# Optimization experiments

Measured on AMD Instinct MI355X. Metric: run time of the kernel, lower is better.

The kernel has to match this reference:

```python
import jax, jax.numpy as jnp
import numpy as np

N = 1024      # num_features
H = 256       # num_hidden_features
E = 64        # embedding_size
HD = 64       # hidden_size
B = 8192


def setup_inputs() -> dict:
    key = jax.random.key(0)
    ks = jax.random.split(key, 7)
    glorot_e = (2.0 / (N + E)) ** 0.5
    glorot_w = (2.0 / (2 * E + HD)) ** 0.5
    glorot_u = (2.0 / (HD + 1)) ** 0.5
    return {
        "values": jax.random.uniform(ks[0], (B, N), dtype=jnp.float32),
        "feat_emb": jax.random.normal(ks[1], (N, E), dtype=jnp.float32) * glorot_e,
        "hid_emb": jax.random.normal(ks[2], (H, E), dtype=jnp.float32) * glorot_e,
        "W_w": jax.random.normal(ks[3], (2 * E, HD), dtype=jnp.float32) * glorot_w,
        "b_w": jnp.zeros((HD,), dtype=jnp.float32),
        "W_u": jax.random.normal(ks[4], (HD, 1), dtype=jnp.float32) * glorot_u,
        "mask": jax.random.bernoulli(ks[5], 0.5, (N, N + H)),
    }


def _forward(values, feat_emb, hid_emb, W_w, b_w, W_u, mask):
    # full embedding table over extended vocab: [M, E], M = N + H
    full = jnp.concatenate([feat_emb, hid_emb], axis=0)
    # Dense w applied to concat([feat_i, full_j]) == split-matmul, avoids [N,M,2E]
    W1, W2 = W_w[:E], W_w[E:]                      # each [E, HD]
    a = feat_emb @ W1                              # [N, HD]
    b = full @ W2                                  # [M, HD]
    h = jnp.tanh(a[:, None, :] + b[None, :, :] + b_w)  # [N, M, HD]
    score = jnp.squeeze(h @ W_u, axis=-1)          # [N, M]
    score = jnp.where(mask, jnp.exp(score), 0.0)
    score_sum = jnp.sum(score, axis=1, keepdims=True)
    score_sum = jnp.where(score_sum == 0, 1.0, score_sum)
    attention_weights = score / score_sum          # [N, M]
    context = attention_weights @ full             # [N, E]
    return values @ context                        # [B, E]


def reference(values, feat_emb, hid_emb, W_w, b_w, W_u, mask):
    return _forward(values, feat_emb, hid_emb, W_w, b_w, W_u, mask)
```

## Files before the change

### kernel.cpp

```cpp
#include <hip/hip_runtime.h>
#include <hip/hip_bf16.h>

#define NF   1024
#define NHID 256
#define NJ   1280
#define ED   64
#define BATCH 8192

#define K2E   2.8853900817779268f
#define LOG2E 1.4426950408889634f

__device__ __forceinline__ float exp2_fast(float x) {
    float r;
    asm("v_exp_f32 %0, %1" : "=v"(r) : "v"(x));
    return r;
}

__global__ __launch_bounds__(256) void prep_kernel(
    const float* __restrict__ feat, const float* __restrict__ hid,
    const float* __restrict__ Ww, const float* __restrict__ bw,
    const float* __restrict__ Wu,
    float* __restrict__ Ap, float* __restrict__ BvT, float* __restrict__ swu)
{
    __shared__ __align__(16) float in_s[64][64];
    __shared__ __align__(16) float tout[64][65];
    const int tid = threadIdx.x;
    const int b   = blockIdx.x;
    const bool isA = (b < 16);
    const int e  = tid & 63;
    const int wv = tid >> 6;

    if (b == 0 && tid < 64) {
        float s = Wu[tid];
        #pragma unroll
        for (int off = 32; off > 0; off >>= 1) s += __shfl_down(s, off);
        if (tid == 0) swu[0] = s * LOG2E;
    }

    const float* W = isA ? Ww : (Ww + 4096);
    float wcol[64];
    #pragma unroll
    for (int k = 0; k < 64; k++) wcol[k] = W[k * 64 + e];
    const float bias = isA ? 0.f : bw[e];

    const int bb = isA ? b : (b - 16);
    const float* src = isA ? (feat + (size_t)bb * 4096)
                     : (bb < 16 ? (feat + (size_t)bb * 4096)
                                : (hid + (size_t)(bb - 16) * 4096));
    #pragma unroll
    for (int s = 0; s < 4; s++)
        ((float4*)&in_s[0][0])[tid + s * 256] = ((const float4*)src)[tid + s * 256];
    __syncthreads();

    float acc[16];
    #pragma unroll
    for (int r = 0; r < 16; r++) acc[r] = bias;
    for (int k4 = 0; k4 < 64; k4 += 4) {
        #pragma unroll
        for (int r = 0; r < 16; r++) {
            float4 iv = *(const float4*)&in_s[wv * 16 + r][k4];
            acc[r] += iv.x*wcol[k4+0] + iv.y*wcol[k4+1] + iv.z*wcol[k4+2] + iv.w*wcol[k4+3];
        }
    }

    if (isA) {
        #pragma unroll
        for (int r = 0; r < 16; r++)
            Ap[(size_t)(b * 64 + wv * 16 + r) * 64 + e] = acc[r] * K2E;
    } else {
        #pragma unroll
        for (int r = 0; r < 16; r++) tout[wv * 16 + r][e] = acc[r] * K2E;
        __syncthreads();
        const int j0 = bb * 64;
        #pragma unroll
        for (int q = 0; q < 4; q++) {
            float4 v;
            v.x = tout[wv * 16 + q * 4 + 0][e];
            v.y = tout[wv * 16 + q * 4 + 1][e];
            v.z = tout[wv * 16 + q * 4 + 2][e];
            v.w = tout[wv * 16 + q * 4 + 3][e];
            *(float4*)&BvT[(size_t)e * NJ + j0 + wv * 16 + q * 4] = v;
        }
    }
}

__global__ __launch_bounds__(256) void score_kernel(
    const float* __restrict__ Wu, const float* __restrict__ Ap,
    const float* __restrict__ BvT, const float* __restrict__ swu,
    const void* __restrict__ maskp, float* __restrict__ sc)
{
    __shared__ int mtype_s;
    const int tid = threadIdx.x;
    const int iq  = blockIdx.x / 5;
    const int jc  = blockIdx.x - iq * 5;
    const int i0  = iq * 4;
    const int j   = jc * 256 + tid;

    if (tid < 64) {
        const unsigned int* mw = (const unsigned int*)maskp;
        unsigned int w = mw[tid];
        unsigned long long notf = __ballot(w != 0u && w != 0x3F800000u);
        unsigned long long gt1  = __ballot(w > 1u);
        if (tid == 0) mtype_s = (notf == 0ull) ? 2 : ((gt1 == 0ull) ? 1 : 0);
    }
    __syncthreads();

    const float* a0p = Ap + (size_t)(i0 + 0) * 64;
    const float* a1p = Ap + (size_t)(i0 + 1) * 64;
    const float* a2p = Ap + (size_t)(i0 + 2) * 64;
    const float* a3p = Ap + (size_t)(i0 + 3) * 64;
    const float* bp  = BvT + j;

    float acc0 = 0.f, acc1 = 0.f, acc2 = 0.f, acc3 = 0.f;
    #pragma unroll 8
    for (int e = 0; e < 64; e++) {
        float b  = bp[(size_t)e * NJ];
        float wu = Wu[e];
        float t, r;
        t = a0p[e] + b; r = __builtin_amdgcn_rcpf(exp2_fast(t) + 1.f); acc0 = fmaf(wu, r, acc0);
        t = a1p[e] + b; r = __builtin_amdgcn_rcpf(exp2_fast(t) + 1.f); acc1 = fmaf(wu, r, acc1);
        t = a2p[e] + b; r = __builtin_amdgcn_rcpf(exp2_fast(t) + 1.f); acc2 = fmaf(wu, r, acc2);
        t = a3p[e] + b; r = __builtin_amdgcn_rcpf(exp2_fast(t) + 1.f); acc3 = fmaf(wu, r, acc3);
    }

    const float SwuL = swu[0];
    const int mtype = mtype_s;
    const unsigned char* m8  = (const unsigned char*)maskp;
    const unsigned int*  m32 = (const unsigned int*)maskp;
    const float*         mfl = (const float*)maskp;
    float av[4] = {acc0, acc1, acc2, acc3};
    #pragma unroll
    for (int i = 0; i < 4; i++) {
        size_t off = (size_t)(i0 + i) * NJ + j;
        bool bm;
        if (mtype == 0)      bm = m8[off]  != 0;
        else if (mtype == 1) bm = m32[off] != 0u;
        else                 bm = mfl[off] != 0.f;
        sc[off] = bm ? exp2_fast(fmaf(-K2E, av[i], SwuL)) : 0.f;
    }
}

__global__ __launch_bounds__(256) void ctx_kernel(
    const float* __restrict__ feat, const float* __restrict__ hid,
    const float* __restrict__ sc, float* __restrict__ ctx)
{
    __shared__ __align__(16) float sc_s[2][NJ];
    __shared__ __align__(16) float red[2][16][64];
    __shared__ float ssum_s[2];
    const int tid = threadIdx.x;
    const int i0  = blockIdx.x * 2;

    #pragma unroll
    for (int rep = 0; rep < 3; rep++) {
        int idx = tid + rep * 256;
        if (idx < 640) {
            int i  = idx / 320;
            int jq = idx - i * 320;
            *(float4*)&sc_s[i][jq * 4] = *(const float4*)&sc[(size_t)(i0 + i) * NJ + jq * 4];
        }
    }
    __syncthreads();
    if (tid < 128) {
        int i = tid >> 6, e = tid & 63;
        float s = 0.f;
        #pragma unroll
        for (int g = 0; g < 20; g++) s += sc_s[i][e + g * 64];
        #pragma unroll
        for (int off = 32; off > 0; off >>= 1) s += __shfl_down(s, off);
        if (e == 0) ssum_s[i] = (s == 0.f) ? 1.f : s;
    }

    const int jg = tid >> 4;
    const int e4 = (tid & 15) * 4;
    float4 c0 = {0.f,0.f,0.f,0.f}, c1 = {0.f,0.f,0.f,0.f};
    for (int it = 0; it < 80; it++) {
        int j = it * 16 + jg;
        const float* fr = (j < NF) ? (feat + (size_t)j * 64)
                                   : (hid  + (size_t)(j - NF) * 64);
        float4 f = *(const float4*)(fr + e4);
        float w0 = sc_s[0][j], w1 = sc_s[1][j];
        c0.x += w0*f.x; c0.y += w0*f.y; c0.z += w0*f.z; c0.w += w0*f.w;
        c1.x += w1*f.x; c1.y += w1*f.y; c1.z += w1*f.z; c1.w += w1*f.w;
    }
    *(float4*)&red[0][jg][e4] = c0;
    *(float4*)&red[1][jg][e4] = c1;
    __syncthreads();
    if (tid < 128) {
        int half = tid >> 6, e = tid & 63;
        float v = 0.f;
        #pragma unroll
        for (int g = 0; g < 16; g++) v += red[half][g][e];
        ctx[(size_t)(i0 + half) * 64 + e] = v / ssum_s[half];
    }
}

__global__ __launch_bounds__(256) void out_mm_kernel(
    const float* __restrict__ values, const float* __restrict__ ctxp,
    float* __restrict__ dst, int atomic_mode)
{
    __shared__ __align__(16) float vsT[64 * 64];
    __shared__ __align__(16) float cs[64][64];
    const int tid = threadIdx.x;
    const int rt  = blockIdx.x >> 3;
    const int kq  = blockIdx.x & 7;
    const int r0  = rt * 64;
    const int tr  = tid >> 4;
    const int tc4 = (tid & 15) * 4;

    float acc[4][4];
    #pragma unroll
    for (int a = 0; a < 4; a++)
        #pragma unroll
        for (int b = 0; b < 4; b++) acc[a][b] = 0.f;

    for (int ch = 0; ch < 2; ch++) {
        const int k0 = kq * 128 + ch * 64;
        __syncthreads();
        #pragma unroll
        for (int s = 0; s < 4; s++) {
            int t   = tid + s * 256;
            int r   = t >> 4;
            int kk4 = (t & 15) * 4;
            float4 g = *(const float4*)&values[(size_t)(r0 + r) * NF + k0 + kk4];
            int p  = (((r >> 2) + (t & 15)) & 15) * 4 + (r & 3);
            vsT[(kk4 + 0) * 64 + p] = g.x;
            vsT[(kk4 + 1) * 64 + p] = g.y;
            vsT[(kk4 + 2) * 64 + p] = g.z;
            vsT[(kk4 + 3) * 64 + p] = g.w;
        }
        #pragma unroll
        for (int s = 0; s < 4; s++) {
            int t  = tid + s * 256;
            int kk = t >> 4;
            int c4 = (t & 15) * 4;
            *(float4*)&cs[kk][c4] = *(const float4*)&ctxp[(size_t)(k0 + kk) * ED + c4];
        }
        __syncthreads();
        #pragma unroll 8
        for (int k = 0; k < 64; k++) {
            float4 av = *(const float4*)&vsT[k * 64 + (((tr + (k >> 2)) & 15) << 2)];
            float4 bv = *(const float4*)&cs[k][tc4];
            acc[0][0] += av.x*bv.x; acc[0][1] += av.x*bv.y; acc[0][2] += av.x*bv.z; acc[0][3] += av.x*bv.w;
            acc[1][0] += av.y*bv.x; acc[1][1] += av.y*bv.y; acc[1][2] += av.y*bv.z; acc[1][3] += av.y*bv.w;
            acc[2][0] += av.z*bv.x; acc[2][1] += av.z*bv.y; acc[2][2] += av.z*bv.z; acc[2][3] += av.z*bv.w;
            acc[3][0] += av.w*bv.x; acc[3][1] += av.w*bv.y; acc[3][2] += av.w*bv.z; acc[3][3] += av.w*bv.w;
        }
    }
    if (atomic_mode) {
        #pragma unroll
        for (int i2 = 0; i2 < 4; i2++) {
            int r = r0 + tr * 4 + i2;
            float* op = dst + (size_t)r * ED + tc4;
            unsafeAtomicAdd(op + 0, acc[i2][0]);
            unsafeAtomicAdd(op + 1, acc[i2][1]);
            unsafeAtomicAdd(op + 2, acc[i2][2]);
            unsafeAtomicAdd(op + 3, acc[i2][3]);
        }
    } else {
        #pragma unroll
        for (int i2 = 0; i2 < 4; i2++) {
            int r = r0 + tr * 4 + i2;
            float* op = dst + ((size_t)kq * BATCH + r) * ED + tc4;
            *(float4*)op = make_float4(acc[i2][0], acc[i2][1], acc[i2][2], acc[i2][3]);
        }
    }
}

__global__ __launch_bounds__(256) void reduce8_kernel(
    const float* __restrict__ part, float* __restrict__ out)
{
    const size_t S = (size_t)BATCH * ED / 4;
    size_t idx = (size_t)blockIdx.x * 256 + threadIdx.x;
    const float4* p = (const float4*)part;
    float4 r = {0.f, 0.f, 0.f, 0.f};
    #pragma unroll
    for (int q = 0; q < 8; q++) {
        float4 a = p[idx + (size_t)q * S];
        r.x += a.x; r.y += a.y; r.z += a.z; r.w += a.w;
    }
    ((float4*)out)[idx] = r;
}

extern "C" void kernel_launch(void* const* d_in, const int* in_sizes, int n_in,
                              void* d_out, int out_size, void* d_ws, size_t ws_size,
                              hipStream_t stream) {
    const float* values = (const float*)d_in[0];
    const float* feat   = (const float*)d_in[1];
    const float* hid    = (const float*)d_in[2];
    const float* Ww     = (const float*)d_in[3];
    const float* bw     = (const float*)d_in[4];
    const float* Wu     = (const float*)d_in[5];
    const void*  mask   = d_in[6];
    float* out = (float*)d_out;

    float* Ap   = (float*)d_ws;
    float* BvT  = Ap + (size_t)NF * 64;
    float* ctx  = BvT + (size_t)ED * NJ;
    float* swu  = ctx + (size_t)NF * 64;
    float* sc   = swu + 64;
    float* part = sc + (size_t)NF * NJ;
    const size_t need = ((size_t)NF*64 + (size_t)ED*NJ + (size_t)NF*64 + 64
                         + (size_t)NF*NJ + (size_t)8*BATCH*ED) * sizeof(float);
    const bool wsmode = ws_size >= need;

    hipLaunchKernelGGL(prep_kernel, dim3(36), dim3(256), 0, stream,
                       feat, hid, Ww, bw, Wu, Ap, BvT, swu);
    hipLaunchKernelGGL(score_kernel, dim3(1280), dim3(256), 0, stream,
                       Wu, Ap, BvT, swu, mask, sc);
    hipLaunchKernelGGL(ctx_kernel, dim3(512), dim3(256), 0, stream,
                       feat, hid, sc, ctx);
    if (wsmode) {
        hipLaunchKernelGGL(out_mm_kernel, dim3(1024), dim3(256), 0, stream,
                           values, ctx, part, 0);
        hipLaunchKernelGGL(reduce8_kernel, dim3(BATCH * ED / 4 / 256), dim3(256), 0, stream,
                           part, out);
    } else {
        hipMemsetAsync(d_out, 0, (size_t)BATCH * ED * sizeof(float), stream);
        hipLaunchKernelGGL(out_mm_kernel, dim3(1024), dim3(256), 0, stream,
                           values, ctx, out, 1);
    }
}
```

Baseline: 146.1 us.

## Retile output matmul to 256x64 blocks with 8x8 register tiles and atomic split-K

The final values@context matmul now uses 256-row tiles with a 64-wide K slice per block and 8x8 per-thread register accumulators, up from 64 rows and 4x4. The split-K partial buffer and separate reduce kernel are removed. Partial sums go straight into the zeroed output with atomic adds across 16 K-splits. This aims to raise arithmetic intensity and drop the extra partial write/read pass and one launch. In exchange it issues more atomics, needs 80KB of shared memory per block (lower occupancy), and uses more registers.

```diff
diff --git a/kernel.cpp b/kernel.cpp
--- a/kernel.cpp
+++ b/kernel.cpp
@@ -196,89 +196,68 @@
 
 __global__ __launch_bounds__(256) void out_mm_kernel(
     const float* __restrict__ values, const float* __restrict__ ctxp,
-    float* __restrict__ dst, int atomic_mode)
-{
-    __shared__ __align__(16) float vsT[64 * 64];
+    float* __restrict__ out)
+{
+    __shared__ __align__(16) float vsT[64 * 256];
     __shared__ __align__(16) float cs[64][64];
     const int tid = threadIdx.x;
-    const int rt  = blockIdx.x >> 3;
-    const int kq  = blockIdx.x & 7;
-    const int r0  = rt * 64;
-    const int tr  = tid >> 4;
-    const int tc4 = (tid & 15) * 4;
-
-    float acc[4][4];
-    #pragma unroll
-    for (int a = 0; a < 4; a++)
-        #pragma unroll
-        for (int b = 0; b < 4; b++) acc[a][b] = 0.f;
-
-    for (int ch = 0; ch < 2; ch++) {
-        const int k0 = kq * 128 + ch * 64;
-        __syncthreads();
-        #pragma unroll
-        for (int s = 0; s < 4; s++) {
-            int t   = tid + s * 256;
-            int r   = t >> 4;
-            int kk4 = (t & 15) * 4;
-            float4 g = *(const float4*)&values[(size_t)(r0 + r) * NF + k0 + kk4];
-            int p  = (((r >> 2) + (t & 15)) & 15) * 4 + (r & 3);
-            vsT[(kk4 + 0) * 64 + p] = g.x;
-            vsT[(kk4 + 1) * 64 + p] = g.y;
-            vsT[(kk4 + 2) * 64 + p] = g.z;
-            vsT[(kk4 + 3) * 64 + p] = g.w;
-        }
-        #pragma unroll
-        for (int s = 0; s < 4; s++) {
-            int t  = tid + s * 256;
-            int kk = t >> 4;
-            int c4 = (t & 15) * 4;
-            *(float4*)&cs[kk][c4] = *(const float4*)&ctxp[(size_t)(k0 + kk) * ED + c4];
-        }
-        __syncthreads();
-        #pragma unroll 8
-        for (int k = 0; k < 64; k++) {
-            float4 av = *(const float4*)&vsT[k * 64 + (((tr + (k >> 2)) & 15) << 2)];
-            float4 bv = *(const float4*)&cs[k][tc4];
-            acc[0][0] += av.x*bv.x; acc[0][1] += av.x*bv.y; acc[0][2] += av.x*bv.z; acc[0][3] += av.x*bv.w;
-            acc[1][0] += av.y*bv.x; acc[1][1] += av.y*bv.y; acc[1][2] += av.y*bv.z; acc[1][3] += av.y*bv.w;
-            acc[2][0] += av.z*bv.x; acc[2][1] += av.z*bv.y; acc[2][2] += av.z*bv.z; acc[2][3] += av.z*bv.w;
-            acc[3][0] += av.w*bv.x; acc[3][1] += av.w*bv.y; acc[3][2] += av.w*bv.z; acc[3][3] += av.w*bv.w;
-        }
-    }
-    if (atomic_mode) {
-        #pragma unroll
-        for (int i2 = 0; i2 < 4; i2++) {
-            int r = r0 + tr * 4 + i2;
-            float* op = dst + (size_t)r * ED + tc4;
-            unsafeAtomicAdd(op + 0, acc[i2][0]);
-            unsafeAtomicAdd(op + 1, acc[i2][1]);
-            unsafeAtomicAdd(op + 2, acc[i2][2]);
-            unsafeAtomicAdd(op + 3, acc[i2][3]);
-        }
-    } else {
-        #pragma unroll
-        for (int i2 = 0; i2 < 4; i2++) {
-            int r = r0 + tr * 4 + i2;
-            float* op = dst + ((size_t)kq * BATCH + r) * ED + tc4;
-            *(float4*)op = make_float4(acc[i2][0], acc[i2][1], acc[i2][2], acc[i2][3]);
-        }
-    }
-}
-
-__global__ __launch_bounds__(256) void reduce8_kernel(
-    const float* __restrict__ part, float* __restrict__ out)
-{
-    const size_t S = (size_t)BATCH * ED / 4;
-    size_t idx = (size_t)blockIdx.x * 256 + threadIdx.x;
-    const float4* p = (const float4*)part;
-    float4 r = {0.f, 0.f, 0.f, 0.f};
-    #pragma unroll
-    for (int q = 0; q < 8; q++) {
-        float4 a = p[idx + (size_t)q * S];
-        r.x += a.x; r.y += a.y; r.z += a.z; r.w += a.w;
-    }
-    ((float4*)out)[idx] = r;
+    const int rt  = blockIdx.x >> 4;
+    const int kq  = blockIdx.x & 15;
+    const int r0  = rt * 256;
+    const int k0  = kq * 64;
+    const int rg  = tid >> 3;
+    const int c8  = (tid & 7) * 8;
+
+    #pragma unroll
+    for (int s = 0; s < 16; s++) {
+        int t  = tid + s * 256;
+        int r  = t >> 4;
+        int kc = t & 15;
+        float4 g = *(const float4*)&values[(size_t)(r0 + r) * NF + k0 + kc * 4];
+        int p = ((((r >> 3) + kc) & 31) << 3) + (r & 7);
+        vsT[(kc * 4 + 0) * 256 + p] = g.x;
+        vsT[(kc * 4 + 1) * 256 + p] = g.y;
+        vsT[(kc * 4 + 2) * 256 + p] = g.z;
+        vsT[(kc * 4 + 3) * 256 + p] = g.w;
+    }
+    #pragma unroll
+    for (int s = 0; s < 4; s++) {
+        int t  = tid + s * 256;
+        int kk = t >> 4;
+        int c4 = (t & 15) * 4;
+        *(float4*)&cs[kk][c4] = *(const float4*)&ctxp[(size_t)(k0 + kk) * ED + c4];
+    }
+    __syncthreads();
+
+    float acc[8][8];
+    #pragma unroll
+    for (int a = 0; a < 8; a++)
+        #pragma unroll
+        for (int b = 0; b < 8; b++) acc[a][b] = 0.f;
+
+    #pragma unroll 4
+    for (int k = 0; k < 64; k++) {
+        int pb = (((rg + (k >> 2)) & 31) << 3);
+        float4 a0 = *(const float4*)&vsT[k * 256 + pb];
+        float4 a1 = *(const float4*)&vsT[k * 256 + pb + 4];
+        float4 b0 = *(const float4*)&cs[k][c8];
+        float4 b1 = *(const float4*)&cs[k][c8 + 4];
+        float av[8] = {a0.x,a0.y,a0.z,a0.w,a1.x,a1.y,a1.z,a1.w};
+        float bv[8] = {b0.x,b0.y,b0.z,b0.w,b1.x,b1.y,b1.z,b1.w};
+        #pragma unroll
+        for (int ri = 0; ri < 8; ri++)
+            #pragma unroll
+            for (int ci = 0; ci < 8; ci++)
+                acc[ri][ci] += av[ri] * bv[ci];
+    }
+
+    #pragma unroll
+    for (int ri = 0; ri < 8; ri++) {
+        float* op = out + (size_t)(r0 + rg * 8 + ri) * ED + c8;
+        #pragma unroll
+        for (int ci = 0; ci < 8; ci++)
+            unsafeAtomicAdd(op + ci, acc[ri][ci]);
+    }
 }
 
 extern "C" void kernel_launch(void* const* d_in, const int* in_sizes, int n_in,
@@ -298,25 +277,14 @@
     float* ctx  = BvT + (size_t)ED * NJ;
     float* swu  = ctx + (size_t)NF * 64;
     float* sc   = swu + 64;
-    float* part = sc + (size_t)NF * NJ;
-    const size_t need = ((size_t)NF*64 + (size_t)ED*NJ + (size_t)NF*64 + 64
-                         + (size_t)NF*NJ + (size_t)8*BATCH*ED) * sizeof(float);
-    const bool wsmode = ws_size >= need;
-
+
+    hipMemsetAsync(d_out, 0, (size_t)BATCH * ED * sizeof(float), stream);
     hipLaunchKernelGGL(prep_kernel, dim3(36), dim3(256), 0, stream,
                        feat, hid, Ww, bw, Wu, Ap, BvT, swu);
     hipLaunchKernelGGL(score_kernel, dim3(1280), dim3(256), 0, stream,
                        Wu, Ap, BvT, swu, mask, sc);
     hipLaunchKernelGGL(ctx_kernel, dim3(512), dim3(256), 0, stream,
                        feat, hid, sc, ctx);
-    if (wsmode) {
-        hipLaunchKernelGGL(out_mm_kernel, dim3(1024), dim3(256), 0, stream,
-                           values, ctx, part, 0);
-        hipLaunchKernelGGL(reduce8_kernel, dim3(BATCH * ED / 4 / 256), dim3(256), 0, stream,
-                           part, out);
-    } else {
-        hipMemsetAsync(d_out, 0, (size_t)BATCH * ED * sizeof(float), stream);
-        hipLaunchKernelGGL(out_mm_kernel, dim3(1024), dim3(256), 0, stream,
-                           values, ctx, out, 1);
-    }
-}
+    hipLaunchKernelGGL(out_mm_kernel, dim3(512), dim3(256), 0, stream,
+                       values, ctx, out);
+}
```

After: 361.5 us. +147.5%, slower.
